# Kernel tuning notes

Hardware: AMD Instinct MI355X
Metric: run time of the kernel (lower is better)

The kernel has to match this reference:

```python
import jax, jax.numpy as jnp
import numpy as np

B, S, D = 8, 1024, 1024
H, DK, DV = 16, 64, 64
OUT = 64  # out_size; W_o output dim = OUT * H = 1024


def setup_inputs() -> dict:
    key = jax.random.key(0)
    ks = jax.random.split(key, 8)
    queries = jax.random.normal(ks[0], (B, S, D), dtype=jnp.float32)
    keys = jax.random.normal(ks[1], (B, S, D), dtype=jnp.float32)
    values = jax.random.normal(ks[2], (B, S, D), dtype=jnp.float32)
    # Linear weights stored as [in, out] (no bias per bias=False)
    Wq = jax.random.normal(ks[3], (D, DK * H), dtype=jnp.float32) * 0.02
    Wk = jax.random.normal(ks[4], (D, DK * H), dtype=jnp.float32) * 0.02
    Wv = jax.random.normal(ks[5], (D, DV * H), dtype=jnp.float32) * 0.02
    Wo = jax.random.normal(ks[6], (DV * H, OUT * H), dtype=jnp.float32) * 0.02
    valid_lens = jax.random.randint(ks[7], (B,), 1, S + 1, dtype=jnp.int32)
    return {"queries": queries, "keys": keys, "values": values,
            "Wq": Wq, "Wk": Wk, "Wv": Wv, "Wo": Wo, "valid_lens": valid_lens}


def reference(queries, keys, values, Wq, Wk, Wv, Wo, valid_lens):
    b, s, _ = queries.shape
    # projections + transpose_qkv: [B,S,H*dh] -> [B,H,S,dh]
    q = (queries @ Wq).reshape(b, s, H, DK).transpose(0, 2, 1, 3)
    k = (keys @ Wk).reshape(b, keys.shape[1], H, DK).transpose(0, 2, 1, 3)
    v = (values @ Wv).reshape(b, values.shape[1], H, DV).transpose(0, 2, 1, 3)
    scale = DK ** 0.5  # epsilon = 0.0
    scores = jnp.einsum('bhqd,bhkd->bhqk', q, k) / scale
    # valid_lens masking on last axis: masked entries set to -1e6 (not -inf)
    kv_len = k.shape[2]
    mask = jnp.arange(kv_len)[None, None, None, :] < valid_lens[:, None, None, None]
    scores = jnp.where(mask, scores, -1e6)
    attn = jax.nn.softmax(scores, axis=-1)  # dropout p=0.0 -> identity
    out = jnp.einsum('bhqk,bhkd->bhqd', attn, v)
    # transpose_output: [B,H,S,dv] -> [B,S,H*dv]
    out = out.transpose(0, 2, 1, 3).reshape(b, s, H * DV)
    return out @ Wo
```

## Files before the change

### kernel.cpp

```cpp
#include <hip/hip_runtime.h>
#include <hip/hip_bf16.h>
#include <stdint.h>

typedef __bf16 bf16_t;
typedef __bf16 bf16x8 __attribute__((ext_vector_type(8)));
typedef float f32x4 __attribute__((ext_vector_type(4)));

#define B_  8
#define S_  1024
#define D_  1024
#define H_  16
#define DH_ 64

static __device__ __forceinline__ f32x4 mfma_bf16(bf16x8 a, bf16x8 b, f32x4 c) {
  return __builtin_amdgcn_mfma_f32_16x16x32_bf16(a, b, c, 0, 0, 0);
}

#define GLOAD_LDS16(g, l)                                                     \
  __builtin_amdgcn_global_load_lds(                                           \
      (const __attribute__((address_space(1))) void*)(g),                     \
      (__attribute__((address_space(3))) void*)(l), 16, 0, 0)

__global__ __launch_bounds__(256) void transpose4(
    const float* __restrict__ w0, const float* __restrict__ w1,
    const float* __restrict__ w2, const float* __restrict__ w3,
    bf16_t* __restrict__ t0, bf16_t* __restrict__ t1,
    bf16_t* __restrict__ t2, bf16_t* __restrict__ t3)
{
  __shared__ float tile[64][65];
  const float* src; bf16_t* dst;
  switch (blockIdx.z) {
    case 0: src = w0; dst = t0; break;
    case 1: src = w1; dst = t1; break;
    case 2: src = w2; dst = t2; break;
    default: src = w3; dst = t3; break;
  }
  const int tx = threadIdx.x & 63;
  const int ty = threadIdx.x >> 6;
  const int c0 = blockIdx.x * 64, r0 = blockIdx.y * 64;
#pragma unroll
  for (int r = ty; r < 64; r += 4)
    tile[r][tx] = src[(size_t)(r0 + r) * 1024 + c0 + tx];
  __syncthreads();
#pragma unroll
  for (int r = ty; r < 64; r += 4)
    dst[(size_t)(c0 + r) * 1024 + r0 + tx] = (bf16_t)tile[tx][r];
}

__global__ __launch_bounds__(256) void convert_qkv(
    const float* __restrict__ q, const float* __restrict__ k,
    const float* __restrict__ v,
    bf16_t* __restrict__ qo, bf16_t* __restrict__ ko, bf16_t* __restrict__ vo)
{
  const float* src; bf16_t* dst;
  switch (blockIdx.y) {
    case 0: src = q; dst = qo; break;
    case 1: src = k; dst = ko; break;
    default: src = v; dst = vo; break;
  }
  const size_t i = ((size_t)blockIdx.x * 256 + threadIdx.x) * 8;
  float4 a = *(const float4*)(src + i);
  float4 b = *(const float4*)(src + i + 4);
  bf16x8 o;
  o[0] = (bf16_t)a.x; o[1] = (bf16_t)a.y; o[2] = (bf16_t)a.z; o[3] = (bf16_t)a.w;
  o[4] = (bf16_t)b.x; o[5] = (bf16_t)b.y; o[6] = (bf16_t)b.z; o[7] = (bf16_t)b.w;
  *(bf16x8*)(dst + i) = o;
}

__global__ __launch_bounds__(256) void transposeV(
    const bf16_t* __restrict__ src, bf16_t* __restrict__ dst)
{
  __shared__ bf16_t t[64 * 72];
  const size_t base = (size_t)blockIdx.y * (64 * 1024);
  const int s0 = blockIdx.x * 64;
#pragma unroll
  for (int it = 0; it < 2; ++it) {
    const int c = it * 256 + threadIdx.x;
    const int r = c >> 3, col8 = (c & 7) * 8;
    bf16x8 v = *(const bf16x8*)(src + base + (size_t)(s0 + r) * 64 + col8);
    *(bf16x8*)(t + r * 72 + col8) = v;
  }
  __syncthreads();
#pragma unroll
  for (int it = 0; it < 2; ++it) {
    const int c = it * 256 + threadIdx.x;
    const int d = c >> 3, sc8 = (c & 7) * 8;
    bf16x8 v;
#pragma unroll
    for (int j = 0; j < 8; ++j) v[j] = t[(sc8 + j) * 72 + d];
    *(bf16x8*)(dst + base + (size_t)d * 1024 + s0 + sc8) = v;
  }
}

template <int MODE>
__device__ __forceinline__ void gemm_core(
    const bf16_t* __restrict__ Ap, const bf16_t* __restrict__ Bp,
    void* __restrict__ Cp, int K, int N)
{
  __shared__ bf16_t As[128 * 32];
  __shared__ bf16_t Bs[128 * 32];

  const int tid  = threadIdx.x;
  const int wv   = tid >> 6;
  const int lane = tid & 63;
  const int wm   = wv >> 1;
  const int wn   = wv & 1;
  const int quad = lane >> 4;
  const int l15  = lane & 15;

  const int tileM = blockIdx.x * 8 + (blockIdx.y & 7);
  const int tileN = blockIdx.y >> 3;

  const int c0  = wv * 128 + lane;
  const int r0  = c0 >> 2;
  const int cl0 = (c0 & 3) << 3;
  const int c1  = c0 + 64;
  const int r1  = c1 >> 2;
  const int cl1 = (c1 & 3) << 3;

  const bf16_t* Arow0 = Ap + (size_t)(tileM * 128 + r0) * K + cl0;
  const bf16_t* Arow1 = Ap + (size_t)(tileM * 128 + r1) * K + cl1;
  const bf16_t* Brow0 = Bp + (size_t)(tileN * 128 + r0) * K + cl0;
  const bf16_t* Brow1 = Bp + (size_t)(tileN * 128 + r1) * K + cl1;

  bf16_t* lA0 = As + (size_t)(wv * 128) * 8;
  bf16_t* lA1 = As + (size_t)(wv * 128 + 64) * 8;
  bf16_t* lB0 = Bs + (size_t)(wv * 128) * 8;
  bf16_t* lB1 = Bs + (size_t)(wv * 128 + 64) * 8;

  f32x4 acc[4][4];
#pragma unroll
  for (int mi = 0; mi < 4; ++mi)
#pragma unroll
    for (int ni = 0; ni < 4; ++ni)
      acc[mi][ni] = (f32x4){0.f, 0.f, 0.f, 0.f};

  for (int k0 = 0; k0 < K; k0 += 32) {
    __syncthreads();
    GLOAD_LDS16(Arow0 + k0, lA0);
    GLOAD_LDS16(Arow1 + k0, lA1);
    GLOAD_LDS16(Brow0 + k0, lB0);
    GLOAD_LDS16(Brow1 + k0, lB1);
    __syncthreads();

    bf16x8 af[4], bfr[4];
#pragma unroll
    for (int mi = 0; mi < 4; ++mi)
      af[mi] = *(const bf16x8*)(As + (wm * 64 + mi * 16 + l15) * 32 + quad * 8);
#pragma unroll
    for (int ni = 0; ni < 4; ++ni)
      bfr[ni] = *(const bf16x8*)(Bs + (wn * 64 + ni * 16 + l15) * 32 + quad * 8);
#pragma unroll
    for (int mi = 0; mi < 4; ++mi)
#pragma unroll
      for (int ni = 0; ni < 4; ++ni)
        acc[mi][ni] = mfma_bf16(af[mi], bfr[ni], acc[mi][ni]);
  }

#pragma unroll
  for (int mi = 0; mi < 4; ++mi) {
#pragma unroll
    for (int ni = 0; ni < 4; ++ni) {
#pragma unroll
      for (int r = 0; r < 4; ++r) {
        const int row = tileM * 128 + wm * 64 + mi * 16 + quad * 4 + r;
        const int col = tileN * 128 + wn * 64 + ni * 16 + l15;
        if (MODE == 0) {
          ((float*)Cp)[(size_t)row * N + col] = acc[mi][ni][r];
        } else {
          const int b = row >> 10, s = row & 1023;
          const int h = col >> 6,  d = col & 63;
          ((bf16_t*)Cp)[(((size_t)(b * H_ + h) << 10) | s) * DH_ + d] =
              (bf16_t)acc[mi][ni][r];
        }
      }
    }
  }
}

__global__ __launch_bounds__(256) void gemm_proj(
    const bf16_t* __restrict__ A0, const bf16_t* __restrict__ A1, const bf16_t* __restrict__ A2,
    const bf16_t* __restrict__ B0, const bf16_t* __restrict__ B1, const bf16_t* __restrict__ B2,
    bf16_t* __restrict__ C0, bf16_t* __restrict__ C1, bf16_t* __restrict__ C2)
{
  const bf16_t* Ap; const bf16_t* Bp; bf16_t* Cp;
  if (blockIdx.z == 0)      { Ap = A0; Bp = B0; Cp = C0; }
  else if (blockIdx.z == 1) { Ap = A1; Bp = B1; Cp = C1; }
  else                      { Ap = A2; Bp = B2; Cp = C2; }
  gemm_core<1>(Ap, Bp, (void*)Cp, 1024, 1024);
}

__global__ __launch_bounds__(256) void gemm_out(
    const bf16_t* __restrict__ Ap, const bf16_t* __restrict__ Bp,
    float* __restrict__ Cp)
{
  gemm_core<0>(Ap, Bp, (void*)Cp, 1024, 1024);
}

__global__ __launch_bounds__(256) void attn64(
    const bf16_t* __restrict__ Q,
    const bf16_t* __restrict__ Kv,
    const bf16_t* __restrict__ Vt,
    const int* __restrict__ valid_lens,
    bf16_t* __restrict__ O)
{
  const int h  = blockIdx.x;
  const int qt = blockIdx.y;
  const int b  = blockIdx.z;
  const int tid  = threadIdx.x;
  const int wave = tid >> 6;
  const int lane = tid & 63;
  const int quad = lane >> 4;
  const int l15  = lane & 15;

  const int L   = valid_lens[b];
  const int nkt = (L + 63) >> 6;

  const size_t base = ((size_t)(b * H_ + h)) * S_ * DH_;
  const bf16_t* Qp = Q  + base;
  const bf16_t* Kp = Kv + base;
  const bf16_t* Vp = Vt + base;

  __shared__ bf16_t KsA[64 * 32];
  __shared__ bf16_t KsB[64 * 32];
  __shared__ bf16_t VsA[64 * 32];
  __shared__ bf16_t VsB[64 * 32];
  __shared__ bf16_t Pb[4][16 * 72];
  bf16_t* const Pw = &Pb[wave][0];

  const int sr = tid >> 2;
  const int sj = (tid & 3) << 3;
  const int ldsOff = (wave * 64) * 8;

  const int qrow = qt * 64 + wave * 16 + l15;
  const bf16x8 qf0 = *(const bf16x8*)(Qp + (size_t)qrow * DH_ + quad * 8);
  const bf16x8 qf1 = *(const bf16x8*)(Qp + (size_t)qrow * DH_ + 32 + quad * 8);

  f32x4 o[4];
  float lsum[4];
#pragma unroll
  for (int r = 0; r < 4; ++r) {
    o[r] = (f32x4){0.f, 0.f, 0.f, 0.f};
    lsum[r] = 0.f;
  }

  for (int kt = 0; kt < nkt; ++kt) {
    const int k0 = kt * 64;

    __syncthreads();
    GLOAD_LDS16(Kp + (size_t)(k0 + sr) * DH_ + sj,      KsA + ldsOff);
    GLOAD_LDS16(Kp + (size_t)(k0 + sr) * DH_ + 32 + sj, KsB + ldsOff);
    GLOAD_LDS16(Vp + (size_t)sr * S_ + k0 + sj,         VsA + ldsOff);
    GLOAD_LDS16(Vp + (size_t)sr * S_ + k0 + 32 + sj,    VsB + ldsOff);
    __syncthreads();

    f32x4 sc[4];
#pragma unroll
    for (int n16 = 0; n16 < 4; ++n16) {
      const int row = (n16 * 16 + l15) * 32 + quad * 8;
      bf16x8 kf0 = *(const bf16x8*)(KsA + row);
      bf16x8 kf1 = *(const bf16x8*)(KsB + row);
      f32x4 s = (f32x4){0.f, 0.f, 0.f, 0.f};
      s = mfma_bf16(qf0, kf0, s);
      s = mfma_bf16(qf1, kf1, s);
      sc[n16] = s;
    }

    if (k0 + 64 <= L) {
#pragma unroll
      for (int n16 = 0; n16 < 4; ++n16) {
#pragma unroll
        for (int r = 0; r < 4; ++r) {
          const float p = __expf(sc[n16][r] * 0.125f);
          lsum[r] += p;
          Pw[(quad * 4 + r) * 72 + n16 * 16 + l15] = (bf16_t)p;
        }
      }
    } else {
#pragma unroll
      for (int n16 = 0; n16 < 4; ++n16) {
        const bool valid = (k0 + n16 * 16 + l15) < L;
#pragma unroll
        for (int r = 0; r < 4; ++r) {
          const float p = valid ? __expf(sc[n16][r] * 0.125f) : 0.f;
          lsum[r] += p;
          Pw[(quad * 4 + r) * 72 + n16 * 16 + l15] = (bf16_t)p;
        }
      }
    }

    const bf16x8 pf0 = *(const bf16x8*)(Pw + l15 * 72 + quad * 8);
    const bf16x8 pf1 = *(const bf16x8*)(Pw + l15 * 72 + 32 + quad * 8);
#pragma unroll
    for (int dt = 0; dt < 4; ++dt) {
      const int row = (dt * 16 + l15) * 32 + quad * 8;
      bf16x8 vf0 = *(const bf16x8*)(VsA + row);
      bf16x8 vf1 = *(const bf16x8*)(VsB + row);
      o[dt] = mfma_bf16(pf0, vf0, o[dt]);
      o[dt] = mfma_bf16(pf1, vf1, o[dt]);
    }
  }

  float inv[4];
#pragma unroll
  for (int r = 0; r < 4; ++r) {
    float t = lsum[r];
    t += __shfl_xor(t, 1, 64);
    t += __shfl_xor(t, 2, 64);
    t += __shfl_xor(t, 4, 64);
    t += __shfl_xor(t, 8, 64);
    inv[r] = 1.f / t;
  }
  const int qout = qt * 64 + wave * 16 + quad * 4;
#pragma unroll
  for (int dt = 0; dt < 4; ++dt) {
#pragma unroll
    for (int r = 0; r < 4; ++r) {
      const float v = o[dt][r] * inv[r];
      O[((size_t)(b * S_ + qout + r)) * (H_ * DH_) + h * DH_ + dt * 16 + l15] = (bf16_t)v;
    }
  }
}

extern "C" void kernel_launch(void* const* d_in, const int* in_sizes, int n_in,
                              void* d_out, int out_size, void* d_ws, size_t ws_size,
                              hipStream_t stream) {
  const float* queries = (const float*)d_in[0];
  const float* keys    = (const float*)d_in[1];
  const float* values  = (const float*)d_in[2];
  const float* Wq      = (const float*)d_in[3];
  const float* Wk      = (const float*)d_in[4];
  const float* Wv      = (const float*)d_in[5];
  const float* Wo      = (const float*)d_in[6];
  const int* valid_lens = (const int*)d_in[7];
  float* out = (float*)d_out;

  bf16_t* ws = (bf16_t*)d_ws;
  const size_t MB = 1024 * 1024;
  bf16_t* WqT = ws + 0 * MB;
  bf16_t* WkT = ws + 1 * MB;
  bf16_t* WvT = ws + 2 * MB;
  bf16_t* WoT = ws + 3 * MB;
  bf16_t* Qc  = ws + 4 * MB;
  bf16_t* Kc  = ws + 12 * MB;
  bf16_t* Vc  = ws + 20 * MB;
  bf16_t* Qb  = ws + 28 * MB;
  bf16_t* Kb  = ws + 36 * MB;
  bf16_t* Vb  = ws + 44 * MB;
  bf16_t* VbT = ws + 52 * MB;
  bf16_t* Ab  = ws + 60 * MB;

  transpose4<<<dim3(16, 16, 4), 256, 0, stream>>>(Wq, Wk, Wv, Wo, WqT, WkT, WvT, WoT);

  convert_qkv<<<dim3(4096, 3), 256, 0, stream>>>(queries, keys, values, Qc, Kc, Vc);

  gemm_proj<<<dim3(8, 64, 3), 256, 0, stream>>>(Qc, Kc, Vc,
                                                WqT, WkT, WvT,
                                                Qb, Kb, Vb);

  transposeV<<<dim3(16, 128), 256, 0, stream>>>(Vb, VbT);

  attn64<<<dim3(16, 16, 8), 256, 0, stream>>>(Qb, Kb, VbT, valid_lens, Ab);

  gemm_out<<<dim3(8, 64, 1), 256, 0, stream>>>(Ab, WoT, out);
}
```

Before: 295.6 us.

## Triple-buffer GEMM LDS with larger 256x128x64 tiles and XOR swizzle

Rewrites the shared GEMM core to use 256x128 block tiles with BK=64, eight waves, and a three-stage ring of LDS buffers in dynamic shared memory. Global-to-LDS loads for tile t+2 are issued before computing tile t, with explicit vmcnt waits, and an XOR swizzle on LDS columns avoids bank conflicts. The goal is to hide global load latency and cut the per-iteration synchronisation of the old single-buffered 128x128x32 loop. In exchange it uses about 144KB of LDS per block, raises s_setprio around the MFMAs, and shrinks the grid to 256 blocks per GEMM.

```diff
diff --git a/kernel.cpp b/kernel.cpp
--- a/kernel.cpp
+++ b/kernel.cpp
@@ -92,13 +92,22 @@
   }
 }
 
+#define BM_G 256
+#define BN_G 128
+#define BK_G 64
+#define KDIM 1024
+#define NK_G (KDIM / BK_G)
+#define ATILE (BM_G * BK_G)
+#define BTILE (BN_G * BK_G)
+#define LDS_BYTES ((3 * (ATILE + BTILE)) * 2)
+
 template <int MODE>
 __device__ __forceinline__ void gemm_core(
     const bf16_t* __restrict__ Ap, const bf16_t* __restrict__ Bp,
-    void* __restrict__ Cp, int K, int N)
-{
-  __shared__ bf16_t As[128 * 32];
-  __shared__ bf16_t Bs[128 * 32];
+    void* __restrict__ Cp, bf16_t* smem)
+{
+  bf16_t* const As = smem;
+  bf16_t* const Bs = smem + 3 * ATILE;
 
   const int tid  = threadIdx.x;
   const int wv   = tid >> 6;
@@ -108,25 +117,24 @@
   const int quad = lane >> 4;
   const int l15  = lane & 15;
 
-  const int tileM = blockIdx.x * 8 + (blockIdx.y & 7);
-  const int tileN = blockIdx.y >> 3;
-
-  const int c0  = wv * 128 + lane;
-  const int r0  = c0 >> 2;
-  const int cl0 = (c0 & 3) << 3;
-  const int c1  = c0 + 64;
-  const int r1  = c1 >> 2;
-  const int cl1 = (c1 & 3) << 3;
-
-  const bf16_t* Arow0 = Ap + (size_t)(tileM * 128 + r0) * K + cl0;
-  const bf16_t* Arow1 = Ap + (size_t)(tileM * 128 + r1) * K + cl1;
-  const bf16_t* Brow0 = Bp + (size_t)(tileN * 128 + r0) * K + cl0;
-  const bf16_t* Brow1 = Bp + (size_t)(tileN * 128 + r1) * K + cl1;
-
-  bf16_t* lA0 = As + (size_t)(wv * 128) * 8;
-  bf16_t* lA1 = As + (size_t)(wv * 128 + 64) * 8;
-  bf16_t* lB0 = Bs + (size_t)(wv * 128) * 8;
-  bf16_t* lB1 = Bs + (size_t)(wv * 128 + 64) * 8;
+  const int tileN = blockIdx.x & 7;
+  const int tileM = blockIdx.x >> 3;
+
+  const int lr  = lane >> 3;
+  const int swz = (((lane & 7) ^ lr) << 3);
+  const bf16_t* gA0 = Ap + (size_t)(tileM * BM_G + wv * 8 + lr) * KDIM + swz;
+  const bf16_t* gB0 = Bp + (size_t)(tileN * BN_G + wv * 8 + lr) * KDIM + swz;
+  const int lA0 = wv * 8 * BK_G;
+  const int lB0 = wv * 8 * BK_G;
+
+#define STAGE_TILE(koff, bA, bB) do {                                          \
+    GLOAD_LDS16(gA0 + (koff),                       As + (bA) + lA0);          \
+    GLOAD_LDS16(gA0 + (size_t)64  * KDIM + (koff),  As + (bA) + lA0 + 64*BK_G); \
+    GLOAD_LDS16(gA0 + (size_t)128 * KDIM + (koff),  As + (bA) + lA0 + 128*BK_G);\
+    GLOAD_LDS16(gA0 + (size_t)192 * KDIM + (koff),  As + (bA) + lA0 + 192*BK_G);\
+    GLOAD_LDS16(gB0 + (koff),                       Bs + (bB) + lB0);          \
+    GLOAD_LDS16(gB0 + (size_t)64  * KDIM + (koff),  Bs + (bB) + lB0 + 64*BK_G); \
+  } while (0)
 
   f32x4 acc[4][4];
 #pragma unroll
@@ -135,27 +143,51 @@
     for (int ni = 0; ni < 4; ++ni)
       acc[mi][ni] = (f32x4){0.f, 0.f, 0.f, 0.f};
 
-  for (int k0 = 0; k0 < K; k0 += 32) {
-    __syncthreads();
-    GLOAD_LDS16(Arow0 + k0, lA0);
-    GLOAD_LDS16(Arow1 + k0, lA1);
-    GLOAD_LDS16(Brow0 + k0, lB0);
-    GLOAD_LDS16(Brow1 + k0, lB1);
-    __syncthreads();
-
-    bf16x8 af[4], bfr[4];
-#pragma unroll
-    for (int mi = 0; mi < 4; ++mi)
-      af[mi] = *(const bf16x8*)(As + (wm * 64 + mi * 16 + l15) * 32 + quad * 8);
-#pragma unroll
-    for (int ni = 0; ni < 4; ++ni)
-      bfr[ni] = *(const bf16x8*)(Bs + (wn * 64 + ni * 16 + l15) * 32 + quad * 8);
-#pragma unroll
-    for (int mi = 0; mi < 4; ++mi)
+  STAGE_TILE(0, 0, 0);
+  STAGE_TILE(BK_G, ATILE, BTILE);
+
+  int cbA = 0, cbB = 0;
+  int sbA = 2 * ATILE, sbB = 2 * BTILE;
+
+  for (int t = 0; t < NK_G; ++t) {
+    if (t + 2 < NK_G) STAGE_TILE((size_t)(t + 2) * BK_G, sbA, sbB);
+
+    if (t < NK_G - 2)       asm volatile("s_waitcnt vmcnt(12)" ::: "memory");
+    else if (t == NK_G - 2) asm volatile("s_waitcnt vmcnt(6)" ::: "memory");
+    else                    asm volatile("s_waitcnt vmcnt(0)" ::: "memory");
+    __builtin_amdgcn_s_barrier();
+    asm volatile("" ::: "memory");
+
+    bf16x8 af[2][4], bfr[2][4];
+#pragma unroll
+    for (int kk = 0; kk < 2; ++kk) {
+      const int sl = (((quad + (kk << 2)) ^ (l15 & 7)) << 3);
+#pragma unroll
+      for (int mi = 0; mi < 4; ++mi)
+        af[kk][mi] = *(const bf16x8*)(As + cbA + (wm * 64 + mi * 16 + l15) * BK_G + sl);
 #pragma unroll
       for (int ni = 0; ni < 4; ++ni)
-        acc[mi][ni] = mfma_bf16(af[mi], bfr[ni], acc[mi][ni]);
-  }
+        bfr[kk][ni] = *(const bf16x8*)(Bs + cbB + (wn * 64 + ni * 16 + l15) * BK_G + sl);
+    }
+    __builtin_amdgcn_s_setprio(1);
+#pragma unroll
+    for (int kk = 0; kk < 2; ++kk)
+#pragma unroll
+      for (int mi = 0; mi < 4; ++mi)
+#pragma unroll
+        for (int ni = 0; ni < 4; ++ni)
+          acc[mi][ni] = mfma_bf16(af[kk][mi], bfr[kk][ni], acc[mi][ni]);
+    __builtin_amdgcn_s_setprio(0);
+
+    asm volatile("" ::: "memory");
+    __builtin_amdgcn_s_barrier();
+
+    cbA += ATILE; if (cbA == 3 * ATILE) cbA = 0;
+    cbB += BTILE; if (cbB == 3 * BTILE) cbB = 0;
+    sbA += ATILE; if (sbA == 3 * ATILE) sbA = 0;
+    sbB += BTILE; if (sbB == 3 * BTILE) sbB = 0;
+  }
+#undef STAGE_TILE
 
 #pragma unroll
   for (int mi = 0; mi < 4; ++mi) {
@@ -163,10 +195,10 @@
     for (int ni = 0; ni < 4; ++ni) {
 #pragma unroll
       for (int r = 0; r < 4; ++r) {
-        const int row = tileM * 128 + wm * 64 + mi * 16 + quad * 4 + r;
-        const int col = tileN * 128 + wn * 64 + ni * 16 + l15;
+        const int row = tileM * BM_G + wm * 64 + mi * 16 + quad * 4 + r;
+        const int col = tileN * BN_G + wn * 64 + ni * 16 + l15;
         if (MODE == 0) {
-          ((float*)Cp)[(size_t)row * N + col] = acc[mi][ni][r];
+          ((float*)Cp)[(size_t)row * 1024 + col] = acc[mi][ni][r];
         } else {
           const int b = row >> 10, s = row & 1023;
           const int h = col >> 6,  d = col & 63;
@@ -178,23 +210,25 @@
   }
 }
 
-__global__ __launch_bounds__(256) void gemm_proj(
+__global__ __launch_bounds__(512, 2) void gemm_proj(
     const bf16_t* __restrict__ A0, const bf16_t* __restrict__ A1, const bf16_t* __restrict__ A2,
     const bf16_t* __restrict__ B0, const bf16_t* __restrict__ B1, const bf16_t* __restrict__ B2,
     bf16_t* __restrict__ C0, bf16_t* __restrict__ C1, bf16_t* __restrict__ C2)
 {
+  extern __shared__ bf16_t smem[];
   const bf16_t* Ap; const bf16_t* Bp; bf16_t* Cp;
   if (blockIdx.z == 0)      { Ap = A0; Bp = B0; Cp = C0; }
   else if (blockIdx.z == 1) { Ap = A1; Bp = B1; Cp = C1; }
   else                      { Ap = A2; Bp = B2; Cp = C2; }
-  gemm_core<1>(Ap, Bp, (void*)Cp, 1024, 1024);
-}
-
-__global__ __launch_bounds__(256) void gemm_out(
+  gemm_core<1>(Ap, Bp, (void*)Cp, smem);
+}
+
+__global__ __launch_bounds__(512, 2) void gemm_out(
     const bf16_t* __restrict__ Ap, const bf16_t* __restrict__ Bp,
     float* __restrict__ Cp)
 {
-  gemm_core<0>(Ap, Bp, (void*)Cp, 1024, 1024);
+  extern __shared__ bf16_t smem[];
+  gemm_core<0>(Ap, Bp, (void*)Cp, smem);
 }
 
 __global__ __launch_bounds__(256) void attn64(
@@ -350,17 +384,22 @@
   bf16_t* VbT = ws + 52 * MB;
   bf16_t* Ab  = ws + 60 * MB;
 
+  (void)hipFuncSetAttribute((const void*)gemm_proj,
+                            hipFuncAttributeMaxDynamicSharedMemorySize, LDS_BYTES);
+  (void)hipFuncSetAttribute((const void*)gemm_out,
+                            hipFuncAttributeMaxDynamicSharedMemorySize, LDS_BYTES);
+
   transpose4<<<dim3(16, 16, 4), 256, 0, stream>>>(Wq, Wk, Wv, Wo, WqT, WkT, WvT, WoT);
 
   convert_qkv<<<dim3(4096, 3), 256, 0, stream>>>(queries, keys, values, Qc, Kc, Vc);
 
-  gemm_proj<<<dim3(8, 64, 3), 256, 0, stream>>>(Qc, Kc, Vc,
-                                                WqT, WkT, WvT,
-                                                Qb, Kb, Vb);
+  gemm_proj<<<dim3(256, 1, 3), 512, LDS_BYTES, stream>>>(Qc, Kc, Vc,
+                                                         WqT, WkT, WvT,
+                                                         Qb, Kb, Vb);
 
   transposeV<<<dim3(16, 128), 256, 0, stream>>>(Vb, VbT);
 
   attn64<<<dim3(16, 16, 8), 256, 0, stream>>>(Qb, Kb, VbT, valid_lens, Ab);
 
-  gemm_out<<<dim3(8, 64, 1), 256, 0, stream>>>(Ab, WoT, out);
-}
+  gemm_out<<<dim3(256, 1, 1), 512, LDS_BYTES, stream>>>(Ab, WoT, out);
+}
```

Measured after the change: 303.9 us. 2.8% more time.
